# Kernel optimization log

Measured on AMD Instinct MI355X. Metric: run time of the kernel, lower is better.

The kernel has to match this reference:

```python
import jax, jax.numpy as jnp
import numpy as np

N_NODES = 4000
N_EDGES = 4000
D_IN = 20      # data_length
HID = 768      # hidden_dim
OUT = 2        # output_dim


def _lin(k, i, o):
    s = 1.0 / np.sqrt(i)
    return jax.random.uniform(k, (i, o), jnp.float32, -s, s)


def setup_inputs() -> dict:
    key = jax.random.key(0)
    ks = jax.random.split(key, 16)
    T = N_NODES + N_EDGES
    data = jax.random.normal(ks[0], (N_NODES, D_IN), jnp.float32)
    data_mask = jnp.ones((N_NODES,), jnp.float32)  # unused by forward, kept for signature fidelity
    e_adj_matrix = jax.random.uniform(ks[1], (T, T), jnp.float32) * (2.0 / T)
    transition = jax.random.randint(ks[2], (2, N_EDGES), 0, N_NODES)
    # exactly N_EDGES ones interleaved among N_NODES zeros
    inx = jnp.concatenate([jnp.ones((N_EDGES,), jnp.int32), jnp.zeros((N_NODES,), jnp.int32)])
    label_inx_positive = jax.random.permutation(ks[3], inx)
    label_inx = jax.random.randint(ks[4], (T,), 0, OUT)
    mask = jax.random.randint(ks[5], (T,), 0, 2).astype(jnp.float32)
    return {
        'data': data, 'data_mask': data_mask, 'e_adj_matrix': e_adj_matrix,
        'transition': transition, 'label_inx_positive': label_inx_positive,
        'label_inx': label_inx, 'mask': mask,
        'mlp_w1': _lin(ks[6], 6 * D_IN, HID), 'mlp_b1': jnp.zeros((HID,), jnp.float32),
        'mlp_w2': _lin(ks[7], HID, HID), 'mlp_b2': jnp.zeros((HID,), jnp.float32),
        'mlp2_w1': _lin(ks[8], D_IN, HID), 'mlp2_b1': jnp.zeros((HID,), jnp.float32),
        'mlp2_w2': _lin(ks[9], HID, HID), 'mlp2_b2': jnp.zeros((HID,), jnp.float32),
        'gcn_w1': _lin(ks[10], HID, HID), 'gcn_b1': jnp.zeros((HID,), jnp.float32),
        'gcn_w2': _lin(ks[11], HID, OUT), 'gcn_b2': jnp.zeros((OUT,), jnp.float32),
    }


def gen_edge2(x, trans):
    # Vectorized Gen_edge2: e1 = [x[t1], x[t0]]; e2 = [x[t0], x[t1]] iff reverse edge exists; e3 = e1 + e2.
    t0, t1 = trans[0], trans[1]
    n = x.shape[0]
    keys = t0 * n + t1
    rkeys = t1 * n + t0
    sk = jnp.sort(keys)
    pos = jnp.clip(jnp.searchsorted(sk, rkeys), 0, sk.shape[0] - 1)
    has_rev = sk[pos] == rkeys  # [E]
    e1 = jnp.concatenate([x[t1], x[t0]], axis=1)  # [E, 2d]
    e2 = jnp.where(has_rev[:, None], jnp.concatenate([x[t0], x[t1]], axis=1), 0.0)
    return jnp.concatenate([e1, e2, e1 + e2], axis=1)  # [E, 6d]


def dataset_cgraph(n_feat, e_feat, e_inx):
    # Vectorized interleave: pull next edge row where e_inx==1, else next node row.
    m = e_inx == 1
    idx_e = jnp.clip(jnp.cumsum(m.astype(jnp.int32)) - 1, 0, e_feat.shape[0] - 1)
    idx_n = jnp.clip(jnp.cumsum((~m).astype(jnp.int32)) - 1, 0, n_feat.shape[0] - 1)
    return jnp.where(m[:, None], e_feat[idx_e], n_feat[idx_n])  # [N+E, H]


def reference(data, data_mask, e_adj_matrix, transition, label_inx_positive,
              label_inx, mask, mlp_w1, mlp_b1, mlp_w2, mlp_b2,
              mlp2_w1, mlp2_b1, mlp2_w2, mlp2_b2,
              gcn_w1, gcn_b1, gcn_w2, gcn_b2):
    e_feat = gen_edge2(data, transition)                              # [E, 120]
    e_feat = jax.nn.relu(e_feat @ mlp_w1 + mlp_b1) @ mlp_w2 + mlp_b2  # [E, H]
    n_feat = jax.nn.relu(data @ mlp2_w1 + mlp2_b1) @ mlp2_w2 + mlp2_b2  # [N, H]
    x = dataset_cgraph(n_feat, e_feat, label_inx_positive)            # [N+E, H]
    # 2-layer GCN (GcnModel assumed standard: relu(A X W1), then A H W2)
    h1 = jax.nn.relu(e_adj_matrix @ (x @ gcn_w1) + gcn_b1)            # [N+E, H]
    logits = e_adj_matrix @ (h1 @ gcn_w2) + gcn_b2                    # [N+E, OUT]
    logp = jax.nn.log_softmax(logits, axis=-1)
    ce = -jnp.take_along_axis(logp, label_inx[:, None], axis=1)[:, 0]
    loss = jnp.sum(ce * mask) / jnp.maximum(jnp.sum(mask), 1.0)
    return logits, loss, h1
```

## Files before the change

kernel.cpp:

```cpp
#include <hip/hip_runtime.h>
#include <hip/hip_bf16.h>

#define N_NODES 4000
#define N_EDGES 4000
#define T_ALL   8000
#define HID     768

typedef __attribute__((ext_vector_type(8))) short bf16x8;
typedef __attribute__((ext_vector_type(4))) short s16x4;
typedef __attribute__((ext_vector_type(4))) float f32x4;

__device__ __forceinline__ short f2bf(float f) {
    union { float f; unsigned u; } a; a.f = f;
    unsigned u = a.u;
    unsigned r = (u + 0x7fffu + ((u >> 16) & 1u)) >> 16;
    return (short)(r & 0xffffu);
}
__device__ __forceinline__ float bf2f(short s) {
    union { unsigned u; float f; } a;
    a.u = ((unsigned)(unsigned short)s) << 16;
    return a.f;
}
__device__ __forceinline__ void gload_lds16(const void* g, void* l) {
    __builtin_amdgcn_global_load_lds(
        (const __attribute__((address_space(1))) void*)g,
        (__attribute__((address_space(3))) void*)l, 16, 0, 0);
}

__device__ __forceinline__ void cvt_job(const float* __restrict__ src,
                                        short* __restrict__ dst, int chunk)
{
    size_t i = (size_t)chunk * 2048 + threadIdx.x * 8;
    float4 v0 = *reinterpret_cast<const float4*>(src + i);
    float4 v1 = *reinterpret_cast<const float4*>(src + i + 4);
    union { bf16x8 v; short s[8]; } u;
    u.s[0] = f2bf(v0.x); u.s[1] = f2bf(v0.y); u.s[2] = f2bf(v0.z); u.s[3] = f2bf(v0.w);
    u.s[4] = f2bf(v1.x); u.s[5] = f2bf(v1.y); u.s[6] = f2bf(v1.z); u.s[7] = f2bf(v1.w);
    *reinterpret_cast<bf16x8*>(dst + i) = u.v;
}

__global__ __launch_bounds__(512, 2) void gemm_ring(
    const short* __restrict__ A, const short* __restrict__ BT,
    short* __restrict__ parts, int M, int K, int lda, int ldbt)
{
    __shared__ __align__(16) short As[4][256 * 32];
    __shared__ __align__(16) short Bs[4][256 * 32];
    const int t    = threadIdx.x;
    const int lane = t & 63;
    const int wv   = t >> 6;
    const int wm   = wv >> 2;
    const int wn   = wv & 3;
    const int lrow = lane & 15;
    const int kgrp = lane >> 4;

    const int nwg  = gridDim.x * gridDim.y * gridDim.z;
    int flat = blockIdx.x + gridDim.x * (blockIdx.y + gridDim.y * blockIdx.z);
    int w    = (flat & 7) * (nwg >> 3) + (flat >> 3);
    const int bx = w % 3;
    int rest = w / 3;
    const int by = rest & 31;
    const int bz = rest >> 5;
    const int bm0 = by << 8;
    const int bn0 = bx << 8;

    const int TC = K >> 5;
    const int Z  = gridDim.z;
    const int q  = TC / Z, r = TC % Z;
    const int nt   = q + (bz < r ? 1 : 0);
    const int kbeg = ((bz < r) ? bz * (q + 1) : r * (q + 1) + (bz - r) * q) << 5;

    auto stageA = [&](int tt) {
        const int k0 = kbeg + (tt << 5);
        short* dst = &As[tt & 3][0];
#pragma unroll
        for (int i = 0; i < 2; ++i) {
            int f = t + (i << 9);
            int row = f >> 2, sl = f & 3;
            int ga = bm0 + row; ga = ga < M ? ga : M - 1;
            gload_lds16(A + (size_t)ga * lda + k0 + ((sl ^ ((row >> 1) & 3)) << 3),
                        dst + f * 8);
        }
    };
    auto stageB = [&](int tt) {
        const int k0 = kbeg + (tt << 5);
        short* dst = &Bs[tt & 3][0];
#pragma unroll
        for (int i = 0; i < 2; ++i) {
            int f = t + (i << 9);
            int row = f >> 2, sl = f & 3;
            gload_lds16(BT + (size_t)(bn0 + row) * ldbt + k0 + ((sl ^ ((row >> 1) & 3)) << 3),
                        dst + f * 8);
        }
    };

    f32x4 acc[8][4];
#pragma unroll
    for (int m = 0; m < 8; ++m)
#pragma unroll
        for (int n = 0; n < 4; ++n) acc[m][n] = (f32x4)(0.0f);

    stageA(0); stageB(0);
    stageA(1); stageB(1);
    stageA(2); stageB(2);
    asm volatile("s_waitcnt vmcnt(4)" ::: "memory");
    __builtin_amdgcn_s_barrier();

    bf16x8 r0A0[4], r0A1[4], r0B[4];
    bf16x8 r1A0[4], r1A1[4], r1B[4];

    {
        const short* Ac = &As[0][0];
        const short* Bc = &Bs[0][0];
#pragma unroll
        for (int m = 0; m < 4; ++m) {
            int rr = (wm << 7) + (m << 4) + lrow;
            r0A0[m] = *reinterpret_cast<const bf16x8*>(
                &Ac[(rr << 5) + ((kgrp ^ ((rr >> 1) & 3)) << 3)]);
        }
#pragma unroll
        for (int n = 0; n < 4; ++n) {
            int rr = (wn << 6) + (n << 4) + lrow;
            r0B[n] = *reinterpret_cast<const bf16x8*>(
                &Bc[(rr << 5) + ((kgrp ^ ((rr >> 1) & 3)) << 3)]);
        }
#pragma unroll
        for (int m = 0; m < 4; ++m) {
            int rr = (wm << 7) + 64 + (m << 4) + lrow;
            r0A1[m] = *reinterpret_cast<const bf16x8*>(
                &Ac[(rr << 5) + ((kgrp ^ ((rr >> 1) & 3)) << 3)]);
        }
    }

#define TILE_STEP(TT, cA0, cA1, cB, nA0, nA1, nB)                              \
    {                                                                          \
        const int _tt = (TT);                                                  \
        if (_tt + 1 < nt) {                                                    \
            const short* An = &As[(_tt + 1) & 3][0];                           \
            const short* Bn = &Bs[(_tt + 1) & 3][0];                           \
            _Pragma("unroll")                                                  \
            for (int m = 0; m < 4; ++m) {                                      \
                int rr = (wm << 7) + (m << 4) + lrow;                          \
                nA0[m] = *reinterpret_cast<const bf16x8*>(                     \
                    &An[(rr << 5) + ((kgrp ^ ((rr >> 1) & 3)) << 3)]);         \
            }                                                                  \
            _Pragma("unroll")                                                  \
            for (int n = 0; n < 4; ++n) {                                      \
                int rr = (wn << 6) + (n << 4) + lrow;                          \
                nB[n] = *reinterpret_cast<const bf16x8*>(                      \
                    &Bn[(rr << 5) + ((kgrp ^ ((rr >> 1) & 3)) << 3)]);         \
            }                                                                  \
            _Pragma("unroll")                                                  \
            for (int m = 0; m < 4; ++m) {                                      \
                int rr = (wm << 7) + 64 + (m << 4) + lrow;                     \
                nA1[m] = *reinterpret_cast<const bf16x8*>(                     \
                    &An[(rr << 5) + ((kgrp ^ ((rr >> 1) & 3)) << 3)]);         \
            }                                                                  \
        }                                                                      \
        if (_tt + 3 < nt) { stageA(_tt + 3); stageB(_tt + 3); }                \
        __builtin_amdgcn_sched_barrier(0);                                     \
        __builtin_amdgcn_s_setprio(1);                                         \
        _Pragma("unroll")                                                      \
        for (int m = 0; m < 4; ++m)                                            \
            _Pragma("unroll")                                                  \
            for (int n = 0; n < 4; ++n)                                        \
                acc[m][n] = __builtin_amdgcn_mfma_f32_16x16x32_bf16(           \
                    cA0[m], cB[n], acc[m][n], 0, 0, 0);                        \
        _Pragma("unroll")                                                      \
        for (int m = 0; m < 4; ++m)                                            \
            _Pragma("unroll")                                                  \
            for (int n = 0; n < 4; ++n)                                        \
                acc[4 + m][n] = __builtin_amdgcn_mfma_f32_16x16x32_bf16(       \
                    cA1[m], cB[n], acc[4 + m][n], 0, 0, 0);                    \
        __builtin_amdgcn_s_setprio(0);                                         \
        if (_tt <= nt - 4) asm volatile("s_waitcnt vmcnt(4)" ::: "memory");    \
        else               asm volatile("s_waitcnt vmcnt(0)" ::: "memory");    \
        __builtin_amdgcn_s_barrier();                                          \
    }

    int tt = 0;
    for (; tt + 1 < nt; tt += 2) {
        TILE_STEP(tt,     r0A0, r0A1, r0B, r1A0, r1A1, r1B);
        TILE_STEP(tt + 1, r1A0, r1A1, r1B, r0A0, r0A1, r0B);
    }
    if (tt < nt) TILE_STEP(tt, r0A0, r0A1, r0B, r1A0, r1A1, r1B);
#undef TILE_STEP

    short* Cp = parts + (size_t)bz * 6144000;
#pragma unroll
    for (int m = 0; m < 8; ++m) {
        int r0 = bm0 + (wm << 7) + (m << 4) + (kgrp << 2);
#pragma unroll
        for (int n = 0; n < 4; ++n) {
            int col = bn0 + (wn << 6) + (n << 4) + lrow;
#pragma unroll
            for (int j = 0; j < 4; ++j) {
                int rr = r0 + j;
                if (rr < M) Cp[(size_t)rr * 768 + col] = f2bf(acc[m][n][j]);
            }
        }
    }
}

template<int BIAS, int RELU, int OUTBF, int AF32, int GAT>
__global__ __launch_bounds__(256) void gemm_bf(
    const void* __restrict__ Av, const short* __restrict__ BT,
    const float* __restrict__ bias, void* __restrict__ Cv,
    int M, int N, int K, int lda, int ldbt, int ldc,
    const int* __restrict__ srcmap)
{
    __shared__ __align__(16) short As[2][128 * 64];
    __shared__ __align__(16) short Bs[2][128 * 64];
    const int t    = threadIdx.x;
    const int lane = t & 63;
    const int wave = t >> 6;
    const int wr   = (wave >> 1) << 6;
    const int wc   = (wave & 1) << 6;
    const int lrow = lane & 15;
    const int kgrp = lane >> 4;
    const int bm0  = blockIdx.y << 7;
    const int bn0  = blockIdx.x << 7;
    const short* Ab = (const short*)Av;
    const float* Af = (const float*)Av;

    const int nk = K >> 6;

    auto stage = [&](int kt, int buf) {
        const int k0 = kt << 6;
#pragma unroll
        for (int i = 0; i < 4; ++i) {
            int f = t + (i << 8);
            int row = f >> 3, slot = f & 7;
            int gb = bn0 + row; gb = (gb < N) ? gb : (N - 1);
            int sr = GAT ? srcmap[gb] : gb;
            gload_lds16(BT + (size_t)sr * ldbt + k0 + ((slot ^ (row & 7)) << 3),
                        &Bs[buf][((i << 8) + (wave << 6)) * 8]);
        }
        if constexpr (!AF32) {
#pragma unroll
            for (int i = 0; i < 4; ++i) {
                int f = t + (i << 8);
                int row = f >> 3, slot = f & 7;
                int ga = bm0 + row; ga = (ga < M) ? ga : (M - 1);
                gload_lds16(Ab + (size_t)ga * lda + k0 + ((slot ^ (row & 7)) << 3),
                            &As[buf][((i << 8) + (wave << 6)) * 8]);
            }
        } else {
#pragma unroll
            for (int i = 0; i < 4; ++i) {
                int f = t + (i << 8);
                int row = f >> 3, c8 = f & 7;
                int ga = bm0 + row; ga = (ga < M) ? ga : (M - 1);
                const float* ap = Af + (size_t)ga * lda + k0 + (c8 << 3);
                float4 v0 = *reinterpret_cast<const float4*>(ap);
                float4 v1 = *reinterpret_cast<const float4*>(ap + 4);
                union { bf16x8 v; short s[8]; } u;
                u.s[0] = f2bf(v0.x); u.s[1] = f2bf(v0.y); u.s[2] = f2bf(v0.z); u.s[3] = f2bf(v0.w);
                u.s[4] = f2bf(v1.x); u.s[5] = f2bf(v1.y); u.s[6] = f2bf(v1.z); u.s[7] = f2bf(v1.w);
                *reinterpret_cast<bf16x8*>(&As[buf][row * 64 + ((c8 ^ (row & 7)) << 3)]) = u.v;
            }
        }
    };

    f32x4 acc[4][4];
#pragma unroll
    for (int m = 0; m < 4; ++m)
#pragma unroll
        for (int n = 0; n < 4; ++n) acc[m][n] = (f32x4)(0.0f);

    auto compute = [&](int buf) {
#pragma unroll
        for (int kk = 0; kk < 2; ++kk) {
            bf16x8 af[4], bfv[4];
#pragma unroll
            for (int m = 0; m < 4; ++m) {
                int rr = wr + m * 16 + lrow;
                af[m] = *reinterpret_cast<const bf16x8*>(
                    &As[buf][rr * 64 + (((kk * 4 + kgrp) ^ (rr & 7)) << 3)]);
            }
#pragma unroll
            for (int n = 0; n < 4; ++n) {
                int rr = wc + n * 16 + lrow;
                bfv[n] = *reinterpret_cast<const bf16x8*>(
                    &Bs[buf][rr * 64 + (((kk * 4 + kgrp) ^ (rr & 7)) << 3)]);
            }
#pragma unroll
            for (int m = 0; m < 4; ++m)
#pragma unroll
                for (int n = 0; n < 4; ++n)
                    acc[m][n] = __builtin_amdgcn_mfma_f32_16x16x32_bf16(
                        af[m], bfv[n], acc[m][n], 0, 0, 0);
        }
    };

    if constexpr (!AF32) {
        stage(0, 0);
        if (nk > 1) stage(1, 1);
        for (int kt = 0; kt < nk - 1; ++kt) {
            asm volatile("s_waitcnt vmcnt(8)" ::: "memory");
            __builtin_amdgcn_s_barrier();
            compute(kt & 1);
            __builtin_amdgcn_s_barrier();
            if (kt + 2 < nk) stage(kt + 2, kt & 1);
        }
        asm volatile("s_waitcnt vmcnt(0)" ::: "memory");
        __builtin_amdgcn_s_barrier();
        compute((nk - 1) & 1);
    } else {
        stage(0, 0);
        __syncthreads();
        int cur = 0;
        for (int kt = 0; kt < nk; ++kt) {
            if (kt + 1 < nk) stage(kt + 1, cur ^ 1);
            compute(cur);
            __syncthreads();
            cur ^= 1;
        }
    }

    short* Cb = (short*)Cv;
    float* Cf = (float*)Cv;
#pragma unroll
    for (int m = 0; m < 4; ++m) {
        int rbase = bm0 + wr + m * 16 + kgrp * 4;
#pragma unroll
        for (int n = 0; n < 4; ++n) {
            int col = bn0 + wc + n * 16 + lrow;
            if (col >= N) continue;
            float bv = BIAS ? bias[col] : 0.0f;
#pragma unroll
            for (int j = 0; j < 4; ++j) {
                int rr = rbase + j;
                if (rr < M) {
                    float v = acc[m][n][j] + bv;
                    if (RELU) v = fmaxf(v, 0.0f);
                    if (OUTBF) Cb[(size_t)rr * ldc + col] = f2bf(v);
                    else       Cf[(size_t)rr * ldc + col] = v;
                }
            }
        }
    }
}

template<int RELU>
__global__ __launch_bounds__(256) void gemm_sel(
    const short* __restrict__ A,
    const short* __restrict__ BT1, const short* __restrict__ BT2,
    const float* __restrict__ bias1, const float* __restrict__ bias2,
    short* __restrict__ C, int K)
{
    __shared__ __align__(16) short As[2][128 * 64];
    __shared__ __align__(16) short Bs[2][128 * 64];
    const int t    = threadIdx.x;
    const int lane = t & 63;
    const int wave = t >> 6;
    const int wr   = (wave >> 1) << 6;
    const int wc   = (wave & 1) << 6;
    const int lrow = lane & 15;
    const int kgrp = lane >> 4;
    const int bm0  = blockIdx.y << 7;
    const int bn0  = blockIdx.x << 7;
    const short* BT   = (bm0 < 4096) ? BT1 : BT2;
    const float* bias = (bm0 < 4096) ? bias1 : bias2;
    const int nk = K >> 6;

    auto stage = [&](int kt, int buf) {
        const int k0 = kt << 6;
#pragma unroll
        for (int i = 0; i < 4; ++i) {
            int f = t + (i << 8);
            int row = f >> 3, slot = f & 7;
            gload_lds16(BT + (size_t)(bn0 + row) * K + k0 + ((slot ^ (row & 7)) << 3),
                        &Bs[buf][((i << 8) + (wave << 6)) * 8]);
        }
#pragma unroll
        for (int i = 0; i < 4; ++i) {
            int f = t + (i << 8);
            int row = f >> 3, slot = f & 7;
            gload_lds16(A + (size_t)(bm0 + row) * K + k0 + ((slot ^ (row & 7)) << 3),
                        &As[buf][((i << 8) + (wave << 6)) * 8]);
        }
    };

    f32x4 acc[4][4];
#pragma unroll
    for (int m = 0; m < 4; ++m)
#pragma unroll
        for (int n = 0; n < 4; ++n) acc[m][n] = (f32x4)(0.0f);

    auto compute = [&](int buf) {
#pragma unroll
        for (int kk = 0; kk < 2; ++kk) {
            bf16x8 af[4], bfv[4];
#pragma unroll
            for (int m = 0; m < 4; ++m) {
                int rr = wr + m * 16 + lrow;
                af[m] = *reinterpret_cast<const bf16x8*>(
                    &As[buf][rr * 64 + (((kk * 4 + kgrp) ^ (rr & 7)) << 3)]);
            }
#pragma unroll
            for (int n = 0; n < 4; ++n) {
                int rr = wc + n * 16 + lrow;
                bfv[n] = *reinterpret_cast<const bf16x8*>(
                    &Bs[buf][rr * 64 + (((kk * 4 + kgrp) ^ (rr & 7)) << 3)]);
            }
#pragma unroll
            for (int m = 0; m < 4; ++m)
#pragma unroll
                for (int n = 0; n < 4; ++n)
                    acc[m][n] = __builtin_amdgcn_mfma_f32_16x16x32_bf16(
                        af[m], bfv[n], acc[m][n], 0, 0, 0);
        }
    };

    stage(0, 0);
    if (nk > 1) stage(1, 1);
    for (int kt = 0; kt < nk - 1; ++kt) {
        asm volatile("s_waitcnt vmcnt(8)" ::: "memory");
        __builtin_amdgcn_s_barrier();
        compute(kt & 1);
        __builtin_amdgcn_s_barrier();
        if (kt + 2 < nk) stage(kt + 2, kt & 1);
    }
    asm volatile("s_waitcnt vmcnt(0)" ::: "memory");
    __builtin_amdgcn_s_barrier();
    compute((nk - 1) & 1);

#pragma unroll
    for (int m = 0; m < 4; ++m) {
        int rbase = bm0 + wr + m * 16 + kgrp * 4;
#pragma unroll
        for (int n = 0; n < 4; ++n) {
            int col = bn0 + wc + n * 16 + lrow;
            float bv = bias[col];
#pragma unroll
            for (int j = 0; j < 4; ++j) {
                float v = acc[m][n][j] + bv;
                if (RELU) v = fmaxf(v, 0.0f);
                C[(size_t)(rbase + j) * 768 + col] = f2bf(v);
            }
        }
    }
}

__global__ __launch_bounds__(256) void prep_all(
    const float* __restrict__ data, const int* __restrict__ trans,
    const float* __restrict__ w1, const float* __restrict__ w2,
    const float* __restrict__ w21, const float* __restrict__ w22,
    const float* __restrict__ gw1, const int* __restrict__ einx,
    short* __restrict__ w1T, short* __restrict__ w2T,
    short* __restrict__ w21T, short* __restrict__ w22T,
    short* __restrict__ gw1T, short* __restrict__ estack,
    int* __restrict__ src,
    const float* __restrict__ cvsrc, short* __restrict__ cvdst,
    int cvoff, int cvcnt)
{
    __shared__ float tile[32][33];
    __shared__ int ibuf[512];
    const int blk = blockIdx.x, tid = threadIdx.x;

    if (blk >= 8497) {
        int jid = blk - 8497;
        if (jid < cvcnt) cvt_job(cvsrc, cvdst, jid + cvoff);
        return;
    }

    if (blk < 2496) {
        if (blk < 384) {
            int i = blk * 256 + tid, n = i >> 7, k = i & 127;
            w1T[i] = (k < 120) ? f2bf(w1[k * 768 + n]) : (short)0;
        } else if (blk < 1344) {
            if (blk < 960) {
                int j = blk - 384, bx = j % 24, by = j / 24;
                int c0 = bx << 5, r0 = by << 5, tx = tid & 31, ty = tid >> 5;
#pragma unroll
                for (int i = ty; i < 32; i += 8)
                    tile[i][tx] = w2[(size_t)(r0 + i) * 768 + c0 + tx];
                __syncthreads();
#pragma unroll
                for (int i = ty; i < 32; i += 8)
                    w2T[(size_t)(c0 + i) * 768 + r0 + tx] = f2bf(tile[tx][i]);
            } else {
                int i = (blk - 960) * 256 + tid, n = i >> 7, k = i & 127;
                w21T[i] = (k < 20) ? f2bf(w21[k * 768 + n]) : (short)0;
            }
        } else if (blk < 1920) {
            int j = blk - 1344, bx = j % 24, by = j / 24;
            int c0 = bx << 5, r0 = by << 5, tx = tid & 31, ty = tid >> 5;
#pragma unroll
            for (int i = ty; i < 32; i += 8)
                tile[i][tx] = w22[(size_t)(r0 + i) * 768 + c0 + tx];
            __syncthreads();
#pragma unroll
            for (int i = ty; i < 32; i += 8)
                w22T[(size_t)(c0 + i) * 768 + r0 + tx] = f2bf(tile[tx][i]);
        } else {
            int j = blk - 1920, bx = j % 24, by = j / 24;
            int c0 = bx << 5, r0 = by << 5, tx = tid & 31, ty = tid >> 5;
#pragma unroll
            for (int i = ty; i < 32; i += 8)
                tile[i][tx] = gw1[(size_t)(r0 + i) * 768 + c0 + tx];
            __syncthreads();
#pragma unroll
            for (int i = ty; i < 32; i += 8)
                gw1T[(size_t)(c0 + i) * 768 + r0 + tx] = f2bf(tile[tx][i]);
        }
    } else if (blk < 6496) {
        int e = blk - 2496;
        int t0 = trans[e], t1 = trans[N_EDGES + e];
        __shared__ int found;
        if (tid == 0) found = 0;
        __syncthreads();
        for (int j = tid; j < N_EDGES; j += 256)
            if (trans[j] == t1 && trans[N_EDGES + j] == t0) found = 1;
        __syncthreads();
        float h = found ? 1.0f : 0.0f;
        short* rp = estack + (size_t)e * 128;
        if (tid < 20) {
            float x0 = data[t0 * 20 + tid];
            float x1 = data[t1 * 20 + tid];
            rp[tid]        = f2bf(x1);
            rp[20 + tid]   = f2bf(x0);
            rp[40 + tid]   = f2bf(h * x0);
            rp[60 + tid]   = f2bf(h * x1);
            rp[80 + tid]   = f2bf(x1 + h * x0);
            rp[100 + tid]  = f2bf(x0 + h * x1);
        } else if (tid < 28) {
            rp[120 + (tid - 20)] = 0;
        }
    } else if (blk < 8496) {
        int i = (blk - 6496) * 256 + tid;
        int r = i >> 7, c = i & 127;
        estack[(size_t)(4096) * 128 + i] = (c < 20) ? f2bf(data[r * 20 + c]) : (short)0;
    } else {
        int* partial = ibuf;
        int* excl    = ibuf + 256;
        int base = tid * 32;
        int cnt = 0;
        for (int i = 0; i < 32; ++i) {
            int idx = base + i;
            if (idx < T_ALL) cnt += (einx[idx] == 1);
        }
        partial[tid] = cnt;
        __syncthreads();
        if (tid == 0) {
            int s = 0;
            for (int i = 0; i < 256; ++i) { excl[i] = s; s += partial[i]; }
        }
        __syncthreads();
        int ce = excl[tid];
        int cn = base - ce;
        for (int i = 0; i < 32; ++i) {
            int idx = base + i;
            if (idx >= T_ALL) break;
            if (einx[idx] == 1) { src[idx] = ce; ce++; }
            else                { src[idx] = 4096 + cn; cn++; }
        }
    }
}

__global__ __launch_bounds__(192) void reduce_h1_hw(
    const short* __restrict__ p, const float* __restrict__ bias,
    const float* __restrict__ w2, float* __restrict__ h1, float* __restrict__ hw,
    int Z)
{
    int r = blockIdx.x, t = threadIdx.x;
    int c0 = t * 4;
    size_t base = (size_t)r * 768 + c0;
    float a[4];
#pragma unroll
    for (int j = 0; j < 4; ++j) a[j] = bias[c0 + j];
    for (int z = 0; z < Z; ++z) {
        s16x4 v = *reinterpret_cast<const s16x4*>(p + (size_t)z * 6144000 + base);
#pragma unroll
        for (int j = 0; j < 4; ++j) a[j] += bf2f(v[j]);
    }
    float d0 = 0.0f, d1 = 0.0f;
    float4 o;
#pragma unroll
    for (int j = 0; j < 4; ++j) {
        float v = fmaxf(a[j], 0.0f);
        ((float*)&o)[j] = v;
        d0 += v * w2[(c0 + j) * 2];
        d1 += v * w2[(c0 + j) * 2 + 1];
    }
    *reinterpret_cast<float4*>(h1 + base) = o;
#pragma unroll
    for (int off = 32; off > 0; off >>= 1) {
        d0 += __shfl_down(d0, off);
        d1 += __shfl_down(d1, off);
    }
    __shared__ float s0[3], s1[3];
    int wvv = t >> 6, ln = t & 63;
    if (ln == 0) { s0[wvv] = d0; s1[wvv] = d1; }
    __syncthreads();
    if (t == 0) {
        hw[r * 2]     = s0[0] + s0[1] + s0[2];
        hw[r * 2 + 1] = s1[0] + s1[1] + s1[2];
    }
}


__global__ void cvt_bf16(const float* __restrict__ in, short* __restrict__ out, int n8)
{
    int i = blockIdx.x * 256 + threadIdx.x;
    if (i >= n8) return;
    float4 v0 = *reinterpret_cast<const float4*>(in + (size_t)i * 8);
    float4 v1 = *reinterpret_cast<const float4*>(in + (size_t)i * 8 + 4);
    union { bf16x8 v; short s[8]; } u;
    u.s[0] = f2bf(v0.x); u.s[1] = f2bf(v0.y); u.s[2] = f2bf(v0.z); u.s[3] = f2bf(v0.w);
    u.s[4] = f2bf(v1.x); u.s[5] = f2bf(v1.y); u.s[6] = f2bf(v1.z); u.s[7] = f2bf(v1.w);
    *reinterpret_cast<bf16x8*>(out + (size_t)i * 8) = u.v;
}

__global__ void gather_x(const short* __restrict__ F2s, const int* __restrict__ src,
                         short* __restrict__ x)
{
    int i = blockIdx.x * 256 + threadIdx.x;
    int r = i / 96, c = i % 96;
    int s = src[r];
    reinterpret_cast<bf16x8*>(x)[i] =
        reinterpret_cast<const bf16x8*>(F2s + (size_t)s * HID)[c];
}

__global__ void h1w2_kernel(const float* __restrict__ h1, const float* __restrict__ w2,
                            float* __restrict__ hw)
{
    int wave = threadIdx.x >> 6, lane = threadIdx.x & 63;
    int row = blockIdx.x * 4 + wave;
    const float* hp = h1 + (size_t)row * HID;
    float a0 = 0.0f, a1 = 0.0f;
    for (int k = lane; k < HID; k += 64) {
        float h = hp[k];
        a0 += h * w2[k * 2];
        a1 += h * w2[k * 2 + 1];
    }
    for (int off = 32; off > 0; off >>= 1) {
        a0 += __shfl_down(a0, off);
        a1 += __shfl_down(a1, off);
    }
    if (lane == 0) { hw[row * 2] = a0; hw[row * 2 + 1] = a1; }
}

__global__ __launch_bounds__(256) void adj_hw_bf(const short* __restrict__ A,
    const float* __restrict__ hw, const float* __restrict__ b2, float* __restrict__ logits)
{
    int row = blockIdx.x;
    const short* ar = A + (size_t)row * T_ALL;
    float a0 = 0.0f, a1 = 0.0f;
    for (int c = threadIdx.x; c < 1000; c += 256) {
        bf16x8 v = *reinterpret_cast<const bf16x8*>(ar + c * 8);
#pragma unroll
        for (int j = 0; j < 8; ++j) {
            float av = bf2f(v[j]);
            int k = c * 8 + j;
            a0 += av * hw[k * 2];
            a1 += av * hw[k * 2 + 1];
        }
    }
    __shared__ float s0[256], s1[256];
    s0[threadIdx.x] = a0; s1[threadIdx.x] = a1;
    __syncthreads();
    for (int o = 128; o > 0; o >>= 1) {
        if (threadIdx.x < o) {
            s0[threadIdx.x] += s0[threadIdx.x + o];
            s1[threadIdx.x] += s1[threadIdx.x + o];
        }
        __syncthreads();
    }
    if (threadIdx.x == 0) {
        logits[row * 2]     = s0[0] + b2[0];
        logits[row * 2 + 1] = s1[0] + b2[1];
    }
}

__global__ __launch_bounds__(256) void adj_hw_f32(const float* __restrict__ A,
    const float* __restrict__ hw, const float* __restrict__ b2, float* __restrict__ logits)
{
    int row = blockIdx.x;
    const float* ar = A + (size_t)row * T_ALL;
    float a0 = 0.0f, a1 = 0.0f;
    for (int k = threadIdx.x; k < T_ALL; k += 256) {
        float v = ar[k];
        a0 += v * hw[k * 2];
        a1 += v * hw[k * 2 + 1];
    }
    __shared__ float s0[256], s1[256];
    s0[threadIdx.x] = a0; s1[threadIdx.x] = a1;
    __syncthreads();
    for (int o = 128; o > 0; o >>= 1) {
        if (threadIdx.x < o) {
            s0[threadIdx.x] += s0[threadIdx.x + o];
            s1[threadIdx.x] += s1[threadIdx.x + o];
        }
        __syncthreads();
    }
    if (threadIdx.x == 0) {
        logits[row * 2]     = s0[0] + b2[0];
        logits[row * 2 + 1] = s1[0] + b2[1];
    }
}

__global__ __launch_bounds__(256) void loss_kernel(const float* __restrict__ logits,
    const int* __restrict__ label, const float* __restrict__ mask, float* __restrict__ outp)
{
    __shared__ float sc[256], sm[256];
    float ac = 0.0f, am = 0.0f;
    for (int i = threadIdx.x; i < T_ALL; i += 256) {
        float l0 = logits[i * 2], l1 = logits[i * 2 + 1];
        float mx = fmaxf(l0, l1);
        float lse = mx + logf(expf(l0 - mx) + expf(l1 - mx));
        float li = label[i] ? l1 : l0;
        ac += (lse - li) * mask[i];
        am += mask[i];
    }
    sc[threadIdx.x] = ac; sm[threadIdx.x] = am;
    __syncthreads();
    for (int o = 128; o > 0; o >>= 1) {
        if (threadIdx.x < o) {
            sc[threadIdx.x] += sc[threadIdx.x + o];
            sm[threadIdx.x] += sm[threadIdx.x + o];
        }
        __syncthreads();
    }
    if (threadIdx.x == 0) *outp = sc[0] / fmaxf(sm[0], 1.0f);
}


extern "C" void kernel_launch(void* const* d_in, const int* in_sizes, int n_in,
                              void* d_out, int out_size, void* d_ws, size_t ws_size,
                              hipStream_t stream)
{
    (void)in_sizes; (void)n_in; (void)out_size;

    const float* data  = (const float*)d_in[0];
    const float* adj   = (const float*)d_in[2];
    const int*   trans = (const int*)d_in[3];
    const int*   einx  = (const int*)d_in[4];
    const int*   label = (const int*)d_in[5];
    const float* mask  = (const float*)d_in[6];
    const float* w1    = (const float*)d_in[7];
    const float* b1    = (const float*)d_in[8];
    const float* w2    = (const float*)d_in[9];
    const float* b2    = (const float*)d_in[10];
    const float* w21   = (const float*)d_in[11];
    const float* b21   = (const float*)d_in[12];
    const float* w22   = (const float*)d_in[13];
    const float* b22   = (const float*)d_in[14];
    const float* gw1   = (const float*)d_in[15];
    const float* gb1   = (const float*)d_in[16];
    const float* gw2   = (const float*)d_in[17];
    const float* gb2   = (const float*)d_in[18];

    char* W = (char*)d_ws;
    short* w1T    = (short*)(W + 0);
    short* w2T    = (short*)(W + 196608);
    short* w21T   = (short*)(W + 1376256);
    short* w22T   = (short*)(W + 1572864);
    short* gw1T   = (short*)(W + 2752512);
    short* estack = (short*)(W + 3932160);
    short* C1s    = (short*)(W + 6029312);
    short* F2s    = (short*)(W + 18612224);
    short* xbuf   = (short*)(W + 31195136);
    int*   src    = (int*)(W + 43499136);

    const bool mid  = (ws_size >= (size_t)140352000);
    const bool big2 = (ws_size >= (size_t)189504000);
    const bool big3 = (ws_size >= (size_t)238656000);

    float* out    = (float*)d_out;
    float* logits = out;
    float* lossp  = out + 16000;
    float* h1     = out + 16001;

    if (big3) {
        short* parts = (short*)(W + 0);
        short* xwT   = (short*)(W + 98304000);
        float* hwbuf = (float*)(W + 110592000);
        short* adjbf = (short*)(W + 110656000);

        prep_all<<<8497 + 31250, 256, 0, stream>>>(data, trans, w1, w2, w21, w22, gw1, einx,
                                                   w1T, w2T, w21T, w22T, gw1T, estack, src,
                                                   adj, adjbf, 0, 31250);
        gemm_sel<1><<<dim3(6, 64), 256, 0, stream>>>(estack, w1T, w21T, b1, b21, C1s, 128);
        gemm_sel<0><<<dim3(6, 64), 256, 0, stream>>>(C1s, w2T, w22T, b2, b22, F2s, 768);
        gemm_bf<0, 0, 1, 0, 1><<<dim3(63, 6), 256, 0, stream>>>(
            gw1T, F2s, nullptr, xwT, 768, 8000, 768, 768, 768, 8000, src);
        gemm_ring<<<dim3(3, 32, 8), 512, 0, stream>>>(adjbf, xwT, parts, 8000, 8000, 8000, 8000);
        reduce_h1_hw<<<8000, 192, 0, stream>>>(parts, gb1, gw2, h1, hwbuf, 8);
        adj_hw_bf<<<8000, 256, 0, stream>>>(adjbf, hwbuf, gb2, logits);
        loss_kernel<<<1, 256, 0, stream>>>(logits, label, mask, lossp);
        return;
    }

    short* adjbf = (short*)W;
    short* xwT;  float* hwbuf;  short* parts = nullptr;
    if (mid) {
        xwT   = (short*)(W + 128000000);
        hwbuf = (float*)(W + 140288000);
        if (big2) parts = (short*)(W + 140352000);
    } else {
        xwT   = (short*)(W + 48425856);
        hwbuf = (float*)(W + 60713856);
    }

    prep_all<<<8497, 256, 0, stream>>>(data, trans, w1, w2, w21, w22, gw1, einx,
                                       w1T, w2T, w21T, w22T, gw1T, estack, src,
                                       nullptr, nullptr, 0, 0);
    gemm_sel<1><<<dim3(6, 64), 256, 0, stream>>>(estack, w1T, w21T, b1, b21, C1s, 128);
    gemm_sel<0><<<dim3(6, 64), 256, 0, stream>>>(C1s, w2T, w22T, b2, b22, F2s, 768);
    gather_x<<<3000, 256, 0, stream>>>(F2s, src, xbuf);
    gemm_bf<0, 0, 1, 0, 0><<<dim3(63, 6), 256, 0, stream>>>(
        gw1T, xbuf, nullptr, xwT, 768, 8000, 768, 768, 768, 8000, nullptr);

    if (mid) {
        cvt_bf16<<<31250, 256, 0, stream>>>(adj, adjbf, 8000000);
        if (big2) {
            gemm_ring<<<dim3(3, 32, 4), 512, 0, stream>>>(adjbf, xwT, parts, 8000, 8000, 8000, 8000);
            reduce_h1_hw<<<8000, 192, 0, stream>>>(parts, gb1, gw2, h1, hwbuf, 4);
        } else {
            gemm_bf<1, 1, 0, 0, 0><<<dim3(6, 63), 256, 0, stream>>>(adjbf, xwT, gb1, h1,
                8000, 768, 8000, 8000, 8000, 768, nullptr);
            h1w2_kernel<<<2000, 256, 0, stream>>>(h1, gw2, hwbuf);
        }
        adj_hw_bf<<<8000, 256, 0, stream>>>(adjbf, hwbuf, gb2, logits);
    } else {
        gemm_bf<1, 1, 0, 1, 0><<<dim3(6, 63), 256, 0, stream>>>(adj, xwT, gb1, h1,
            8000, 768, 8000, 8000, 8000, 768, nullptr);
        h1w2_kernel<<<2000, 256, 0, stream>>>(h1, gw2, hwbuf);
        adj_hw_f32<<<8000, 256, 0, stream>>>(adj, hwbuf, gb2, logits);
    }
    loss_kernel<<<1, 256, 0, stream>>>(logits, label, mask, lossp);
}
```

Baseline: 305.9 us.

## Fuse fp32-to-bf16 adjacency conversion into ring GEMM A-tile staging

Removes the separate pass that converted the fp32 adjacency matrix to bf16. The ring GEMM now loads fp32 rows, converts them in registers and writes swizzled bf16 into LDS, and the logits matvec reads fp32 adjacency directly. This drops a large conversion write/read and lowers the workspace requirement, enabling the split-K path with less memory. The cost is doubled A-read bytes per GEMM pass and synchronous register-staged loads in place of asynchronous direct-to-LDS loads, which may weaken latency hiding.

```diff
diff --git a/kernel.cpp b/kernel.cpp
--- a/kernel.cpp
+++ b/kernel.cpp
@@ -27,20 +27,8 @@
         (__attribute__((address_space(3))) void*)l, 16, 0, 0);
 }
 
-__device__ __forceinline__ void cvt_job(const float* __restrict__ src,
-                                        short* __restrict__ dst, int chunk)
-{
-    size_t i = (size_t)chunk * 2048 + threadIdx.x * 8;
-    float4 v0 = *reinterpret_cast<const float4*>(src + i);
-    float4 v1 = *reinterpret_cast<const float4*>(src + i + 4);
-    union { bf16x8 v; short s[8]; } u;
-    u.s[0] = f2bf(v0.x); u.s[1] = f2bf(v0.y); u.s[2] = f2bf(v0.z); u.s[3] = f2bf(v0.w);
-    u.s[4] = f2bf(v1.x); u.s[5] = f2bf(v1.y); u.s[6] = f2bf(v1.z); u.s[7] = f2bf(v1.w);
-    *reinterpret_cast<bf16x8*>(dst + i) = u.v;
-}
-
 __global__ __launch_bounds__(512, 2) void gemm_ring(
-    const short* __restrict__ A, const short* __restrict__ BT,
+    const float* __restrict__ A, const short* __restrict__ BT,
     short* __restrict__ parts, int M, int K, int lda, int ldbt)
 {
     __shared__ __align__(16) short As[4][256 * 32];
@@ -69,16 +57,31 @@
     const int nt   = q + (bz < r ? 1 : 0);
     const int kbeg = ((bz < r) ? bz * (q + 1) : r * (q + 1) + (bz - r) * q) << 5;
 
+    const int arow = t >> 1;
+    const int kh   = (t & 1) << 4;
+    const int aswz = (arow >> 1) & 3;
+    const int sl0  = kh >> 3;
+
     auto stageA = [&](int tt) {
         const int k0 = kbeg + (tt << 5);
-        short* dst = &As[tt & 3][0];
-#pragma unroll
-        for (int i = 0; i < 2; ++i) {
-            int f = t + (i << 9);
-            int row = f >> 2, sl = f & 3;
-            int ga = bm0 + row; ga = ga < M ? ga : M - 1;
-            gload_lds16(A + (size_t)ga * lda + k0 + ((sl ^ ((row >> 1) & 3)) << 3),
-                        dst + f * 8);
+        short* dst = &As[tt & 3][arow << 5];
+        int ga = bm0 + arow; ga = ga < M ? ga : M - 1;
+        const float* ap = A + (size_t)ga * lda + k0 + kh;
+        {
+            float4 v0 = *reinterpret_cast<const float4*>(ap);
+            float4 v1 = *reinterpret_cast<const float4*>(ap + 4);
+            union { bf16x8 v; short s[8]; } u;
+            u.s[0] = f2bf(v0.x); u.s[1] = f2bf(v0.y); u.s[2] = f2bf(v0.z); u.s[3] = f2bf(v0.w);
+            u.s[4] = f2bf(v1.x); u.s[5] = f2bf(v1.y); u.s[6] = f2bf(v1.z); u.s[7] = f2bf(v1.w);
+            *reinterpret_cast<bf16x8*>(&dst[(sl0 ^ aswz) << 3]) = u.v;
+        }
+        {
+            float4 v2 = *reinterpret_cast<const float4*>(ap + 8);
+            float4 v3 = *reinterpret_cast<const float4*>(ap + 12);
+            union { bf16x8 v; short s[8]; } u;
+            u.s[0] = f2bf(v2.x); u.s[1] = f2bf(v2.y); u.s[2] = f2bf(v2.z); u.s[3] = f2bf(v2.w);
+            u.s[4] = f2bf(v3.x); u.s[5] = f2bf(v3.y); u.s[6] = f2bf(v3.z); u.s[7] = f2bf(v3.w);
+            *reinterpret_cast<bf16x8*>(&dst[((sl0 + 1) ^ aswz) << 3]) = u.v;
         }
     };
     auto stageB = [&](int tt) {
@@ -99,10 +102,11 @@
 #pragma unroll
         for (int n = 0; n < 4; ++n) acc[m][n] = (f32x4)(0.0f);
 
-    stageA(0); stageB(0);
-    stageA(1); stageB(1);
-    stageA(2); stageB(2);
+    stageB(0); stageA(0);
+    stageB(1); stageA(1);
+    stageB(2); stageA(2);
     asm volatile("s_waitcnt vmcnt(4)" ::: "memory");
+    asm volatile("s_waitcnt lgkmcnt(0)" ::: "memory");
     __builtin_amdgcn_s_barrier();
 
     bf16x8 r0A0[4], r0A1[4], r0B[4];
@@ -156,7 +160,7 @@
                     &An[(rr << 5) + ((kgrp ^ ((rr >> 1) & 3)) << 3)]);         \
             }                                                                  \
         }                                                                      \
-        if (_tt + 3 < nt) { stageA(_tt + 3); stageB(_tt + 3); }                \
+        if (_tt + 3 < nt) { stageB(_tt + 3); stageA(_tt + 3); }                \
         __builtin_amdgcn_sched_barrier(0);                                     \
         __builtin_amdgcn_s_setprio(1);                                         \
         _Pragma("unroll")                                                      \
@@ -172,8 +176,9 @@
                 acc[4 + m][n] = __builtin_amdgcn_mfma_f32_16x16x32_bf16(       \
                     cA1[m], cB[n], acc[4 + m][n], 0, 0, 0);                    \
         __builtin_amdgcn_s_setprio(0);                                         \
-        if (_tt <= nt - 4) asm volatile("s_waitcnt vmcnt(4)" ::: "memory");    \
+        if (_tt <= nt - 4) asm volatile("s_waitcnt vmcnt(2)" ::: "memory");    \
         else               asm volatile("s_waitcnt vmcnt(0)" ::: "memory");    \
+        asm volatile("s_waitcnt lgkmcnt(0)" ::: "memory");                     \
         __builtin_amdgcn_s_barrier();                                          \
     }
 
@@ -450,19 +455,11 @@
     short* __restrict__ w1T, short* __restrict__ w2T,
     short* __restrict__ w21T, short* __restrict__ w22T,
     short* __restrict__ gw1T, short* __restrict__ estack,
-    int* __restrict__ src,
-    const float* __restrict__ cvsrc, short* __restrict__ cvdst,
-    int cvoff, int cvcnt)
+    int* __restrict__ src)
 {
     __shared__ float tile[32][33];
     __shared__ int ibuf[512];
     const int blk = blockIdx.x, tid = threadIdx.x;
-
-    if (blk >= 8497) {
-        int jid = blk - 8497;
-        if (jid < cvcnt) cvt_job(cvsrc, cvdst, jid + cvoff);
-        return;
-    }
 
     if (blk < 2496) {
         if (blk < 384) {
@@ -600,18 +597,6 @@
 }
 
 
-__global__ void cvt_bf16(const float* __restrict__ in, short* __restrict__ out, int n8)
-{
-    int i = blockIdx.x * 256 + threadIdx.x;
-    if (i >= n8) return;
-    float4 v0 = *reinterpret_cast<const float4*>(in + (size_t)i * 8);
-    float4 v1 = *reinterpret_cast<const float4*>(in + (size_t)i * 8 + 4);
-    union { bf16x8 v; short s[8]; } u;
-    u.s[0] = f2bf(v0.x); u.s[1] = f2bf(v0.y); u.s[2] = f2bf(v0.z); u.s[3] = f2bf(v0.w);
-    u.s[4] = f2bf(v1.x); u.s[5] = f2bf(v1.y); u.s[6] = f2bf(v1.z); u.s[7] = f2bf(v1.w);
-    *reinterpret_cast<bf16x8*>(out + (size_t)i * 8) = u.v;
-}
-
 __global__ void gather_x(const short* __restrict__ F2s, const int* __restrict__ src,
                          short* __restrict__ x)
 {
@@ -639,38 +624,6 @@
         a1 += __shfl_down(a1, off);
     }
     if (lane == 0) { hw[row * 2] = a0; hw[row * 2 + 1] = a1; }
-}
-
-__global__ __launch_bounds__(256) void adj_hw_bf(const short* __restrict__ A,
-    const float* __restrict__ hw, const float* __restrict__ b2, float* __restrict__ logits)
-{
-    int row = blockIdx.x;
-    const short* ar = A + (size_t)row * T_ALL;
-    float a0 = 0.0f, a1 = 0.0f;
-    for (int c = threadIdx.x; c < 1000; c += 256) {
-        bf16x8 v = *reinterpret_cast<const bf16x8*>(ar + c * 8);
-#pragma unroll
-        for (int j = 0; j < 8; ++j) {
-            float av = bf2f(v[j]);
-            int k = c * 8 + j;
-            a0 += av * hw[k * 2];
-            a1 += av * hw[k * 2 + 1];
-        }
-    }
-    __shared__ float s0[256], s1[256];
-    s0[threadIdx.x] = a0; s1[threadIdx.x] = a1;
-    __syncthreads();
-    for (int o = 128; o > 0; o >>= 1) {
-        if (threadIdx.x < o) {
-            s0[threadIdx.x] += s0[threadIdx.x + o];
-            s1[threadIdx.x] += s1[threadIdx.x + o];
-        }
-        __syncthreads();
-    }
-    if (threadIdx.x == 0) {
-        logits[row * 2]     = s0[0] + b2[0];
-        logits[row * 2 + 1] = s1[0] + b2[1];
-    }
 }
 
 __global__ __launch_bounds__(256) void adj_hw_f32(const float* __restrict__ A,
@@ -763,71 +716,44 @@
     short* xbuf   = (short*)(W + 31195136);
     int*   src    = (int*)(W + 43499136);
 
-    const bool mid  = (ws_size >= (size_t)140352000);
-    const bool big2 = (ws_size >= (size_t)189504000);
-    const bool big3 = (ws_size >= (size_t)238656000);
+    const bool ok = (ws_size >= (size_t)110656000);
 
     float* out    = (float*)d_out;
     float* logits = out;
     float* lossp  = out + 16000;
     float* h1     = out + 16001;
 
-    if (big3) {
+    if (ok) {
         short* parts = (short*)(W + 0);
         short* xwT   = (short*)(W + 98304000);
         float* hwbuf = (float*)(W + 110592000);
-        short* adjbf = (short*)(W + 110656000);
-
-        prep_all<<<8497 + 31250, 256, 0, stream>>>(data, trans, w1, w2, w21, w22, gw1, einx,
-                                                   w1T, w2T, w21T, w22T, gw1T, estack, src,
-                                                   adj, adjbf, 0, 31250);
+
+        prep_all<<<8497, 256, 0, stream>>>(data, trans, w1, w2, w21, w22, gw1, einx,
+                                           w1T, w2T, w21T, w22T, gw1T, estack, src);
         gemm_sel<1><<<dim3(6, 64), 256, 0, stream>>>(estack, w1T, w21T, b1, b21, C1s, 128);
         gemm_sel<0><<<dim3(6, 64), 256, 0, stream>>>(C1s, w2T, w22T, b2, b22, F2s, 768);
         gemm_bf<0, 0, 1, 0, 1><<<dim3(63, 6), 256, 0, stream>>>(
             gw1T, F2s, nullptr, xwT, 768, 8000, 768, 768, 768, 8000, src);
-        gemm_ring<<<dim3(3, 32, 8), 512, 0, stream>>>(adjbf, xwT, parts, 8000, 8000, 8000, 8000);
+        gemm_ring<<<dim3(3, 32, 8), 512, 0, stream>>>(adj, xwT, parts, 8000, 8000, 8000, 8000);
         reduce_h1_hw<<<8000, 192, 0, stream>>>(parts, gb1, gw2, h1, hwbuf, 8);
-        adj_hw_bf<<<8000, 256, 0, stream>>>(adjbf, hwbuf, gb2, logits);
+        adj_hw_f32<<<8000, 256, 0, stream>>>(adj, hwbuf, gb2, logits);
         loss_kernel<<<1, 256, 0, stream>>>(logits, label, mask, lossp);
         return;
     }
 
-    short* adjbf = (short*)W;
-    short* xwT;  float* hwbuf;  short* parts = nullptr;
-    if (mid) {
-        xwT   = (short*)(W + 128000000);
-        hwbuf = (float*)(W + 140288000);
-        if (big2) parts = (short*)(W + 140352000);
-    } else {
-        xwT   = (short*)(W + 48425856);
-        hwbuf = (float*)(W + 60713856);
-    }
+    short* xwT   = (short*)(W + 48425856);
+    float* hwbuf = (float*)(W + 60713856);
 
     prep_all<<<8497, 256, 0, stream>>>(data, trans, w1, w2, w21, w22, gw1, einx,
-                                       w1T, w2T, w21T, w22T, gw1T, estack, src,
-                                       nullptr, nullptr, 0, 0);
+                                       w1T, w2T, w21T, w22T, gw1T, estack, src);
     gemm_sel<1><<<dim3(6, 64), 256, 0, stream>>>(estack, w1T, w21T, b1, b21, C1s, 128);
     gemm_sel<0><<<dim3(6, 64), 256, 0, stream>>>(C1s, w2T, w22T, b2, b22, F2s, 768);
     gather_x<<<3000, 256, 0, stream>>>(F2s, src, xbuf);
     gemm_bf<0, 0, 1, 0, 0><<<dim3(63, 6), 256, 0, stream>>>(
         gw1T, xbuf, nullptr, xwT, 768, 8000, 768, 768, 768, 8000, nullptr);
-
-    if (mid) {
-        cvt_bf16<<<31250, 256, 0, stream>>>(adj, adjbf, 8000000);
-        if (big2) {
-            gemm_ring<<<dim3(3, 32, 4), 512, 0, stream>>>(adjbf, xwT, parts, 8000, 8000, 8000, 8000);
-            reduce_h1_hw<<<8000, 192, 0, stream>>>(parts, gb1, gw2, h1, hwbuf, 4);
-        } else {
-            gemm_bf<1, 1, 0, 0, 0><<<dim3(6, 63), 256, 0, stream>>>(adjbf, xwT, gb1, h1,
-                8000, 768, 8000, 8000, 8000, 768, nullptr);
-            h1w2_kernel<<<2000, 256, 0, stream>>>(h1, gw2, hwbuf);
-        }
-        adj_hw_bf<<<8000, 256, 0, stream>>>(adjbf, hwbuf, gb2, logits);
-    } else {
-        gemm_bf<1, 1, 0, 1, 0><<<dim3(6, 63), 256, 0, stream>>>(adj, xwT, gb1, h1,
-            8000, 768, 8000, 8000, 8000, 768, nullptr);
-        h1w2_kernel<<<2000, 256, 0, stream>>>(h1, gw2, hwbuf);
-        adj_hw_f32<<<8000, 256, 0, stream>>>(adj, hwbuf, gb2, logits);
-    }
+    gemm_bf<1, 1, 0, 1, 0><<<dim3(6, 63), 256, 0, stream>>>(
+        adj, xwT, gb1, h1, 8000, 768, 8000, 8000, 8000, 768, nullptr);
+    h1w2_kernel<<<2000, 256, 0, stream>>>(h1, gw2, hwbuf);
+    adj_hw_f32<<<8000, 256, 0, stream>>>(adj, hwbuf, gb2, logits);
     loss_kernel<<<1, 256, 0, stream>>>(logits, label, mask, lossp);
 }
```

After: 450.5 us. 47.3% more time.

## Use four waves with 128x128 per-wave tiles in ring GEMM

Applied to the files above, without the earlier changes.

The split-K ring GEMM drops from 512 to 256 threads per block, so each of the four waves now computes a 128x128 sub-tile (8x8 MFMA accumulators) instead of 128x64. The hand-written ping-pong register prefetch macro is replaced by a simple loop that waits on vmcnt, barriers, issues the next global-to-LDS stage, then loads fragments and runs the MFMAs. The intent is more operand reuse per wave and fewer LDS reads per MFMA. In exchange the accumulators alone take about 256 VGPRs, occupancy drops to one block per CU, and LDS reads are no longer overlapped with MFMA work.

```diff
diff --git a/kernel.cpp b/kernel.cpp
--- a/kernel.cpp
+++ b/kernel.cpp
@@ -39,7 +39,7 @@
     *reinterpret_cast<bf16x8*>(dst + i) = u.v;
 }
 
-__global__ __launch_bounds__(512, 2) void gemm_ring(
+__global__ __launch_bounds__(256, 1) void gemm_ring(
     const short* __restrict__ A, const short* __restrict__ BT,
     short* __restrict__ parts, int M, int K, int lda, int ldbt)
 {
@@ -48,8 +48,8 @@
     const int t    = threadIdx.x;
     const int lane = t & 63;
     const int wv   = t >> 6;
-    const int wm   = wv >> 2;
-    const int wn   = wv & 3;
+    const int wm   = wv >> 1;
+    const int wn   = wv & 1;
     const int lrow = lane & 15;
     const int kgrp = lane >> 4;
 
@@ -73,8 +73,8 @@
         const int k0 = kbeg + (tt << 5);
         short* dst = &As[tt & 3][0];
 #pragma unroll
-        for (int i = 0; i < 2; ++i) {
-            int f = t + (i << 9);
+        for (int i = 0; i < 4; ++i) {
+            int f = t + (i << 8);
             int row = f >> 2, sl = f & 3;
             int ga = bm0 + row; ga = ga < M ? ga : M - 1;
             gload_lds16(A + (size_t)ga * lda + k0 + ((sl ^ ((row >> 1) & 3)) << 3),
@@ -85,113 +85,66 @@
         const int k0 = kbeg + (tt << 5);
         short* dst = &Bs[tt & 3][0];
 #pragma unroll
-        for (int i = 0; i < 2; ++i) {
-            int f = t + (i << 9);
+        for (int i = 0; i < 4; ++i) {
+            int f = t + (i << 8);
             int row = f >> 2, sl = f & 3;
             gload_lds16(BT + (size_t)(bn0 + row) * ldbt + k0 + ((sl ^ ((row >> 1) & 3)) << 3),
                         dst + f * 8);
         }
     };
 
-    f32x4 acc[8][4];
+    f32x4 acc[8][8];
 #pragma unroll
     for (int m = 0; m < 8; ++m)
 #pragma unroll
-        for (int n = 0; n < 4; ++n) acc[m][n] = (f32x4)(0.0f);
+        for (int n = 0; n < 8; ++n) acc[m][n] = (f32x4)(0.0f);
 
     stageA(0); stageB(0);
     stageA(1); stageB(1);
     stageA(2); stageB(2);
-    asm volatile("s_waitcnt vmcnt(4)" ::: "memory");
-    __builtin_amdgcn_s_barrier();
-
-    bf16x8 r0A0[4], r0A1[4], r0B[4];
-    bf16x8 r1A0[4], r1A1[4], r1B[4];
-
-    {
-        const short* Ac = &As[0][0];
-        const short* Bc = &Bs[0][0];
-#pragma unroll
-        for (int m = 0; m < 4; ++m) {
+
+    for (int tt = 0; tt < nt; ++tt) {
+        int ahead = nt - 1 - tt;
+        if (ahead >= 2)      asm volatile("s_waitcnt vmcnt(16)" ::: "memory");
+        else if (ahead == 1) asm volatile("s_waitcnt vmcnt(8)"  ::: "memory");
+        else                 asm volatile("s_waitcnt vmcnt(0)"  ::: "memory");
+        __builtin_amdgcn_sched_barrier(0);
+        __builtin_amdgcn_s_barrier();
+
+        if (tt + 3 < nt) { stageA(tt + 3); stageB(tt + 3); }
+
+        const short* Ac = &As[tt & 3][0];
+        const short* Bc = &Bs[tt & 3][0];
+        bf16x8 af[8], bfv[8];
+#pragma unroll
+        for (int m = 0; m < 8; ++m) {
             int rr = (wm << 7) + (m << 4) + lrow;
-            r0A0[m] = *reinterpret_cast<const bf16x8*>(
+            af[m] = *reinterpret_cast<const bf16x8*>(
                 &Ac[(rr << 5) + ((kgrp ^ ((rr >> 1) & 3)) << 3)]);
         }
 #pragma unroll
-        for (int n = 0; n < 4; ++n) {
-            int rr = (wn << 6) + (n << 4) + lrow;
-            r0B[n] = *reinterpret_cast<const bf16x8*>(
+        for (int n = 0; n < 8; ++n) {
+            int rr = (wn << 7) + (n << 4) + lrow;
+            bfv[n] = *reinterpret_cast<const bf16x8*>(
                 &Bc[(rr << 5) + ((kgrp ^ ((rr >> 1) & 3)) << 3)]);
         }
-#pragma unroll
-        for (int m = 0; m < 4; ++m) {
-            int rr = (wm << 7) + 64 + (m << 4) + lrow;
-            r0A1[m] = *reinterpret_cast<const bf16x8*>(
-                &Ac[(rr << 5) + ((kgrp ^ ((rr >> 1) & 3)) << 3)]);
-        }
-    }
-
-#define TILE_STEP(TT, cA0, cA1, cB, nA0, nA1, nB)                              \
-    {                                                                          \
-        const int _tt = (TT);                                                  \
-        if (_tt + 1 < nt) {                                                    \
-            const short* An = &As[(_tt + 1) & 3][0];                           \
-            const short* Bn = &Bs[(_tt + 1) & 3][0];                           \
-            _Pragma("unroll")                                                  \
-            for (int m = 0; m < 4; ++m) {                                      \
-                int rr = (wm << 7) + (m << 4) + lrow;                          \
-                nA0[m] = *reinterpret_cast<const bf16x8*>(                     \
-                    &An[(rr << 5) + ((kgrp ^ ((rr >> 1) & 3)) << 3)]);         \
-            }                                                                  \
-            _Pragma("unroll")                                                  \
-            for (int n = 0; n < 4; ++n) {                                      \
-                int rr = (wn << 6) + (n << 4) + lrow;                          \
-                nB[n] = *reinterpret_cast<const bf16x8*>(                      \
-                    &Bn[(rr << 5) + ((kgrp ^ ((rr >> 1) & 3)) << 3)]);         \
-            }                                                                  \
-            _Pragma("unroll")                                                  \
-            for (int m = 0; m < 4; ++m) {                                      \
-                int rr = (wm << 7) + 64 + (m << 4) + lrow;                     \
-                nA1[m] = *reinterpret_cast<const bf16x8*>(                     \
-                    &An[(rr << 5) + ((kgrp ^ ((rr >> 1) & 3)) << 3)]);         \
-            }                                                                  \
-        }                                                                      \
-        if (_tt + 3 < nt) { stageA(_tt + 3); stageB(_tt + 3); }                \
-        __builtin_amdgcn_sched_barrier(0);                                     \
-        __builtin_amdgcn_s_setprio(1);                                         \
-        _Pragma("unroll")                                                      \
-        for (int m = 0; m < 4; ++m)                                            \
-            _Pragma("unroll")                                                  \
-            for (int n = 0; n < 4; ++n)                                        \
-                acc[m][n] = __builtin_amdgcn_mfma_f32_16x16x32_bf16(           \
-                    cA0[m], cB[n], acc[m][n], 0, 0, 0);                        \
-        _Pragma("unroll")                                                      \
-        for (int m = 0; m < 4; ++m)                                            \
-            _Pragma("unroll")                                                  \
-            for (int n = 0; n < 4; ++n)                                        \
-                acc[4 + m][n] = __builtin_amdgcn_mfma_f32_16x16x32_bf16(       \
-                    cA1[m], cB[n], acc[4 + m][n], 0, 0, 0);                    \
-        __builtin_amdgcn_s_setprio(0);                                         \
-        if (_tt <= nt - 4) asm volatile("s_waitcnt vmcnt(4)" ::: "memory");    \
-        else               asm volatile("s_waitcnt vmcnt(0)" ::: "memory");    \
-        __builtin_amdgcn_s_barrier();                                          \
-    }
-
-    int tt = 0;
-    for (; tt + 1 < nt; tt += 2) {
-        TILE_STEP(tt,     r0A0, r0A1, r0B, r1A0, r1A1, r1B);
-        TILE_STEP(tt + 1, r1A0, r1A1, r1B, r0A0, r0A1, r0B);
-    }
-    if (tt < nt) TILE_STEP(tt, r0A0, r0A1, r0B, r1A0, r1A1, r1B);
-#undef TILE_STEP
+        __builtin_amdgcn_s_setprio(1);
+#pragma unroll
+        for (int m = 0; m < 8; ++m)
+#pragma unroll
+            for (int n = 0; n < 8; ++n)
+                acc[m][n] = __builtin_amdgcn_mfma_f32_16x16x32_bf16(
+                    af[m], bfv[n], acc[m][n], 0, 0, 0);
+        __builtin_amdgcn_s_setprio(0);
+    }
 
     short* Cp = parts + (size_t)bz * 6144000;
 #pragma unroll
     for (int m = 0; m < 8; ++m) {
         int r0 = bm0 + (wm << 7) + (m << 4) + (kgrp << 2);
 #pragma unroll
-        for (int n = 0; n < 4; ++n) {
-            int col = bn0 + (wn << 6) + (n << 4) + lrow;
+        for (int n = 0; n < 8; ++n) {
+            int col = bn0 + (wn << 7) + (n << 4) + lrow;
 #pragma unroll
             for (int j = 0; j < 4; ++j) {
                 int rr = r0 + j;
@@ -785,7 +738,7 @@
         gemm_sel<0><<<dim3(6, 64), 256, 0, stream>>>(C1s, w2T, w22T, b2, b22, F2s, 768);
         gemm_bf<0, 0, 1, 0, 1><<<dim3(63, 6), 256, 0, stream>>>(
             gw1T, F2s, nullptr, xwT, 768, 8000, 768, 768, 768, 8000, src);
-        gemm_ring<<<dim3(3, 32, 8), 512, 0, stream>>>(adjbf, xwT, parts, 8000, 8000, 8000, 8000);
+        gemm_ring<<<dim3(3, 32, 8), 256, 0, stream>>>(adjbf, xwT, parts, 8000, 8000, 8000, 8000);
         reduce_h1_hw<<<8000, 192, 0, stream>>>(parts, gb1, gw2, h1, hwbuf, 8);
         adj_hw_bf<<<8000, 256, 0, stream>>>(adjbf, hwbuf, gb2, logits);
         loss_kernel<<<1, 256, 0, stream>>>(logits, label, mask, lossp);
@@ -815,7 +768,7 @@
     if (mid) {
         cvt_bf16<<<31250, 256, 0, stream>>>(adj, adjbf, 8000000);
         if (big2) {
-            gemm_ring<<<dim3(3, 32, 4), 512, 0, stream>>>(adjbf, xwT, parts, 8000, 8000, 8000, 8000);
+            gemm_ring<<<dim3(3, 32, 4), 256, 0, stream>>>(adjbf, xwT, parts, 8000, 8000, 8000, 8000);
             reduce_h1_hw<<<8000, 192, 0, stream>>>(parts, gb1, gw2, h1, hwbuf, 4);
         } else {
             gemm_bf<1, 1, 0, 0, 0><<<dim3(6, 63), 256, 0, stream>>>(adjbf, xwT, gb1, h1,
```

Result: slower. 358.0 us (+17.0%).
